# Performance work log

Hardware: AMD Instinct MI355X
Metric: run time of the kernel (lower is better)

## Reference

```python
import jax, jax.numpy as jnp
import numpy as np

B, S, D_MODEL, N_HEADS = 4, 2048, 512, 2
D4 = D_MODEL * 4            # output dim of quaternion projections (2048)
HD = D4 // N_HEADS          # per-head dim (1024)
EPS = 1e-6


def quat_linear(x, W, b):
    """Hamilton-product quaternion linear.
    x: [..., 4*in_q] (quaternions interleaved r,i,j,k)
    W: [4, out_q, in_q] components (r,i,j,k); b: [4*out_q]
    returns [..., 4*out_q]
    """
    xq = x.reshape(x.shape[:-1] + (-1, 4))
    xr, xi, xj, xk = xq[..., 0], xq[..., 1], xq[..., 2], xq[..., 3]
    Wr, Wi, Wj, Wk = W[0], W[1], W[2], W[3]
    m = lambda a, M: jnp.einsum('...i,oi->...o', a, M)
    o_r = m(xr, Wr) - m(xi, Wi) - m(xj, Wj) - m(xk, Wk)
    o_i = m(xr, Wi) + m(xi, Wr) + m(xj, Wk) - m(xk, Wj)
    o_j = m(xr, Wj) - m(xi, Wk) + m(xj, Wr) + m(xk, Wi)
    o_k = m(xr, Wk) + m(xi, Wj) - m(xj, Wi) + m(xk, Wr)
    out = jnp.stack([o_r, o_i, o_j, o_k], axis=-1)
    return out.reshape(out.shape[:-2] + (-1,)) + b


def setup_inputs() -> dict:
    rng = jax.random.key(0)
    ks = jax.random.split(rng, 12)
    def w(k, out_q, in_q):
        return jax.random.normal(k, (4, out_q, in_q), jnp.float32) * (1.0 / np.sqrt(4.0 * in_q))
    in_q_small = D_MODEL // 4   # q/k/v projections: d_model reals -> d_model quaternions
    in_q_big = D4 // 4          # later projections: 4*d_model reals -> d_model quaternions
    zb = jnp.zeros((D4,), jnp.float32)
    return {
        'query': jax.random.normal(ks[0], (B, S, D_MODEL), jnp.float32),
        'key':   jax.random.normal(ks[1], (B, S, D_MODEL), jnp.float32),
        'value': jax.random.normal(ks[2], (B, S, D_MODEL), jnp.float32),
        'Wq': w(ks[3], D_MODEL, in_q_small), 'bq': zb,
        'Wk': w(ks[4], D_MODEL, in_q_small), 'bk': zb,
        'Wv': w(ks[5], D_MODEL, in_q_small), 'bv': zb,
        'alpha': jax.random.normal(ks[6], (D4,), jnp.float32) * 0.1,
        'Wint': w(ks[7], D_MODEL, in_q_big), 'bint': zb,
        'Wfin': w(ks[8], D_MODEL, in_q_big), 'bfin': zb,
        'Wout': w(ks[9], D_MODEL, in_q_big), 'bout': zb,
    }


def reference(query, key, value, Wq, bq, Wk, bk, Wv, bv, alpha,
              Wint, bint, Wfin, bfin, Wout, bout):
    Q = quat_linear(query, Wq, bq).reshape(B, S, N_HEADS, HD)
    K = quat_linear(key, Wk, bk).reshape(B, S, N_HEADS, HD)
    V = quat_linear(value, Wv, bv).reshape(B, S, N_HEADS, HD)

    # spectral attention: FFT correlation + adaptive spectral filter
    Qf = jnp.fft.fft(Q, axis=1)
    Kf = jnp.fft.fft(K, axis=1)
    corr = Qf * jnp.conj(Kf)                        # [B,S,H,HD] complex64
    freqs = jnp.abs(jnp.fft.fftfreq(S))             # [S]
    phase = jnp.arctan(jnp.log(freqs + EPS))        # [S]
    a = alpha.reshape(N_HEADS, HD)
    filt = jnp.exp(1j * (phase[:, None, None] * a[None, :, :]))  # [S,H,HD]
    attn_w = jnp.fft.ifft(corr * filt[None], axis=1).real        # [B,S,H,HD]
    attn = (attn_w * V).reshape(B, S, -1)           # [B,S,4*d_model]

    attn = quat_linear(attn, Wint, bint)
    attn = quat_linear(attn, Wfin, bfin)
    return quat_linear(attn, Wout, bout)            # [B,S,4*d_model]
```

## Files before the change

kernel.cpp:

```cpp
#include <hip/hip_runtime.h>
#include <hip/hip_bf16.h>
#include <cstdint>

typedef unsigned short u16;
typedef u16  u16x8 __attribute__((ext_vector_type(8)));
typedef short s16x8 __attribute__((ext_vector_type(8)));
typedef float f32x4 __attribute__((ext_vector_type(4)));

#define PI_F 3.14159265358979323846f
#define PD(i) ((i) + 3 * ((i) >> 5))

static __device__ __forceinline__ u16 f2bf(float f) {
    union { float f; unsigned u; } v; v.f = f;
    unsigned r = v.u + 0x7fffu + ((v.u >> 16) & 1u);
    return (u16)(r >> 16);
}
static __device__ __forceinline__ float bf2f(u16 h) {
    union { unsigned u; float f; } v; v.u = ((unsigned)h) << 16;
    return v.f;
}

__device__ __forceinline__ void gl_lds16(const u16* g, u16* l) {
    __builtin_amdgcn_global_load_lds(
        (const __attribute__((address_space(1))) unsigned int*)g,
        (__attribute__((address_space(3))) unsigned int*)l, 16, 0, 0);
}

__device__ __forceinline__ void cvt_body(int blk, const float* __restrict__ in,
                                         u16* __restrict__ o) {
    int i = blk * 256 + threadIdx.x;
    float4 a = ((const float4*)in)[2 * i];
    float4 b = ((const float4*)in)[2 * i + 1];
    u16x8 vv;
    vv[0] = f2bf(a.x); vv[1] = f2bf(a.y); vv[2] = f2bf(a.z); vv[3] = f2bf(a.w);
    vv[4] = f2bf(b.x); vv[5] = f2bf(b.y); vv[6] = f2bf(b.z); vv[7] = f2bf(b.w);
    ((u16x8*)o)[i] = vv;
}

template<int LOGK>
__device__ __forceinline__ void e3_body(int blk, const float* __restrict__ W,
                                        u16* __restrict__ E) {
    const int K = 1 << LOGK;
    int idx = blk * 256 + threadIdx.x;
    int n = idx >> LOGK, k = idx & (K - 1);
    int o = n >> 2, c = n & 3, i = k >> 2, cp = k & 3;
    const int   qm[4][4] = {{0,1,2,3},{1,0,3,2},{2,3,0,1},{3,2,1,0}};
    const float qs[4][4] = {{1.f,-1.f,-1.f,-1.f},{1.f,1.f,1.f,-1.f},
                            {1.f,-1.f,1.f,1.f},{1.f,1.f,-1.f,1.f}};
    int in_q = K >> 2;
    float w = W[(size_t)qm[c][cp] * 512 * in_q + (size_t)o * in_q + i] * qs[c][cp];
    E[idx] = f2bf(w);
}

__device__ __forceinline__ void tabs_body(int blk, float2* __restrict__ gws,
                                          float* __restrict__ ph) {
    int i = blk * 256 + threadIdx.x;
    if (i < 292) {
        int off, denom;
        if (i < 4)       { off = 0;  denom = 16;   }
        else if (i < 36) { off = 4;  denom = 128;  }
        else             { off = 36; denom = 1024; }
        float a = (-PI_F) * (float)(i - off) / (float)denom;
        gws[i] = make_float2(cosf(a), sinf(a));
    }
    if (i <= 1024) {
        ph[i] = atanf(logf((float)i * (1.0f / 2048.0f) + 1e-6f));
    }
}

__global__ __launch_bounds__(256) void fat_prep(
        const float* __restrict__ query, const float* __restrict__ key,
        const float* __restrict__ value, u16* __restrict__ Acvt,
        const float* __restrict__ Wq, const float* __restrict__ Wk,
        const float* __restrict__ Wv, u16* __restrict__ Eq,
        u16* __restrict__ Ek, u16* __restrict__ Ev,
        const float* __restrict__ Wint, const float* __restrict__ Wfin,
        const float* __restrict__ Wout, u16* __restrict__ Eint,
        u16* __restrict__ Efin, u16* __restrict__ Eout,
        float2* __restrict__ gws, float* __restrict__ pht) {
    int b = blockIdx.x;
    if (b < 6144) {
        int ten = b >> 11, r = b & 2047;
        const float* in = (ten == 0) ? query : (ten == 1) ? key : value;
        cvt_body(r, in, Acvt + (size_t)ten * 8192 * 512);
    } else if (b < 18432) {
        int rb = b - 6144;
        int y = rb >> 12, r = rb & 4095;
        e3_body<9>(r, (y == 0) ? Wq : (y == 1) ? Wk : Wv,
                   (y == 0) ? Eq : (y == 1) ? Ek : Ev);
    } else if (b < 67584) {
        int rb = b - 18432;
        int y = rb >> 14, r = rb & 16383;
        e3_body<11>(r, (y == 0) ? Wint : (y == 1) ? Wfin : Wout,
                    (y == 0) ? Eint : (y == 1) ? Efin : Eout);
    } else {
        tabs_body(b - 67584, gws, pht);
    }
}

__global__ __launch_bounds__(256) void matvec_E(const float* __restrict__ v,
                                                const u16* __restrict__ E,
                                                const float* __restrict__ badd,
                                                float* __restrict__ out) {
    int n    = (blockIdx.x * 256 + threadIdx.x) >> 6;
    int lane = threadIdx.x & 63;
    if (n >= 2048) return;
    const u16* row = E + (size_t)n * 2048;
    float s = 0.f;
    for (int j = lane; j < 2048; j += 64) s += v[j] * bf2f(row[j]);
#pragma unroll
    for (int o = 32; o; o >>= 1) s += __shfl_down(s, o, 64);
    if (lane == 0) out[n] = s + badd[n];
}

template<int K, int OUTMODE, int NBY>
__device__ __forceinline__ void gemm_body(int bid, u16* As, u16* Bs,
                                          const u16* __restrict__ A,
                                          const u16* __restrict__ E,
                                          const float* __restrict__ bias,
                                          void* __restrict__ outp) {
    const int t    = threadIdx.x;
    const int lane = t & 63, wave = t >> 6;
    const int wr   = wave >> 1, wc = wave & 1;
    const int lr   = lane & 15, kg = lane >> 4;
    const int l7   = lr & 7;

    constexpr int SPX = (4 * (NBY / 4)) / 8;
    const int xcd = bid & 7, p = bid >> 3;
    const int st  = xcd * SPX + (p >> 4);
    const int w   = p & 15;
    const int bx  = (st & 3) * 4 + (w & 3);
    const int by  = (st >> 2) * 4 + (w >> 2);
    const int m0  = by * 128;
    const int n0  = bx * 128;

    f32x4 acc[4][4];
#pragma unroll
    for (int i = 0; i < 4; ++i)
#pragma unroll
        for (int j = 0; j < 4; ++j) acc[i][j] = (f32x4){0.f, 0.f, 0.f, 0.f};

    const int arow = wr * 64 + lr;
    const int brow = wc * 64 + lr;

    for (int k0 = 0; k0 < K; k0 += 64) {
#pragma unroll
        for (int c = 0; c < 4; ++c) {
            int idx = t + c * 256;
            int row = idx >> 3, sl = idx & 7;
            int gsl = sl ^ (row & 7);
            gl_lds16(A + (size_t)(m0 + row) * K + k0 + gsl * 8, &As[idx * 8]);
            gl_lds16(E + (size_t)(n0 + row) * K + k0 + gsl * 8, &Bs[idx * 8]);
        }
        __syncthreads();
#pragma unroll
        for (int ks = 0; ks < 2; ++ks) {
            const int slot = (ks * 4 + kg) ^ l7;
            s16x8 av[4], bv[4];
#pragma unroll
            for (int mi = 0; mi < 4; ++mi)
                av[mi] = *(const s16x8*)&As[(arow + mi * 16) * 64 + slot * 8];
#pragma unroll
            for (int ni = 0; ni < 4; ++ni)
                bv[ni] = *(const s16x8*)&Bs[(brow + ni * 16) * 64 + slot * 8];
#pragma unroll
            for (int mi = 0; mi < 4; ++mi)
#pragma unroll
                for (int ni = 0; ni < 4; ++ni)
                    acc[mi][ni] = __builtin_amdgcn_mfma_f32_16x16x32_bf16(
                        av[mi], bv[ni], acc[mi][ni], 0, 0, 0);
        }
        __syncthreads();
    }

#pragma unroll
    for (int ni = 0; ni < 4; ++ni) {
        int n = n0 + wc * 64 + ni * 16 + lr;
        float bvl = bias ? bias[n] : 0.0f;
#pragma unroll
        for (int mi = 0; mi < 4; ++mi) {
#pragma unroll
            for (int r = 0; r < 4; ++r) {
                int m = m0 + wr * 64 + mi * 16 + kg * 4 + r;
                float val = acc[mi][ni][r] + bvl;
                if constexpr (OUTMODE == 0) {
                    ((u16*)outp)[(size_t)m * 2048 + n] = f2bf(val);
                } else if constexpr (OUTMODE == 1) {
                    ((float*)outp)[(size_t)m * 2048 + n] = val;
                } else {
                    int b = m >> 11, s = m & 2047;
                    ((u16*)outp)[((size_t)b * 2048 + n) * 2048 + s] = f2bf(val);
                }
            }
        }
    }
}

template<int K, int OUTMODE, int NBY>
__global__ __launch_bounds__(256) void gemm2(const u16* __restrict__ A,
                                             const u16* __restrict__ E,
                                             const float* __restrict__ bias,
                                             void* __restrict__ outp) {
    __shared__ u16 As[128 * 64];
    __shared__ u16 Bs[128 * 64];
    gemm_body<K, OUTMODE, NBY>(blockIdx.x, As, Bs, A, E, bias, outp);
}

__global__ __launch_bounds__(256) void gemm_fatA(const u16* __restrict__ Aq,
                                                 const u16* __restrict__ Eq,
                                                 const float* __restrict__ bq,
                                                 void* __restrict__ Qt,
                                                 const u16* __restrict__ Ak,
                                                 const u16* __restrict__ Ek,
                                                 const float* __restrict__ bk,
                                                 void* __restrict__ Kt,
                                                 const u16* __restrict__ Efin,
                                                 const u16* __restrict__ EintT,
                                                 void* __restrict__ T1T) {
    __shared__ u16 As[128 * 64];
    __shared__ u16 Bs[128 * 64];
    int bid = blockIdx.x;
    if (bid < 256) {
        gemm_body<2048, 2, 16>(bid, As, Bs, Efin, EintT, nullptr, T1T);
    } else {
        int pid = bid - 256;
        if (pid < 1024)
            gemm_body<512, 2, 64>(pid, As, Bs, Aq, Eq, bq, Qt);
        else
            gemm_body<512, 2, 64>(pid - 1024, As, Bs, Ak, Ek, bk, Kt);
    }
}

template<int LH, int OFF>
__device__ __forceinline__ void r8pass(float* re, float* im,
                                       const float2* __restrict__ wt, int t) {
    constexpr int h = 1 << LH;
    __syncthreads();
    const int j  = t & (h - 1);
    const int i0 = ((t >> LH) << (LH + 3)) | j;
    const float2 w = wt[OFF + j];
    const float t2r = w.x * w.x - w.y * w.y;
    const float t2i = 2.f * w.x * w.y;
    const float t1r = t2r * t2r - t2i * t2i;
    const float t1i = 2.f * t2r * t2i;
    const float S = 0.70710678118654752f;
    const float Ac = S * (w.x + w.y);
    const float Bc = S * (w.y - w.x);

    float xr[8], xi[8];
    int p[8];
#pragma unroll
    for (int k = 0; k < 8; ++k) {
        p[k] = PD(i0 + k * h);
        xr[k] = re[p[k]]; xi[k] = im[p[k]];
    }
#pragma unroll
    for (int kp = 0; kp < 8; kp += 2) {
        float tr = t1r * xr[kp + 1] - t1i * xi[kp + 1];
        float ti = t1r * xi[kp + 1] + t1i * xr[kp + 1];
        float ar = xr[kp], ai = xi[kp];
        xr[kp] = ar + tr;     xi[kp] = ai + ti;
        xr[kp + 1] = ar - tr; xi[kp + 1] = ai - ti;
    }
#pragma unroll
    for (int q = 0; q < 2; ++q) {
        int b0 = q * 4;
        {
            float tr = t2r * xr[b0 + 2] - t2i * xi[b0 + 2];
            float ti = t2r * xi[b0 + 2] + t2i * xr[b0 + 2];
            float ar = xr[b0], ai = xi[b0];
            xr[b0] = ar + tr;     xi[b0] = ai + ti;
            xr[b0 + 2] = ar - tr; xi[b0 + 2] = ai - ti;
        }
        {
            float tr = t2i * xr[b0 + 3] + t2r * xi[b0 + 3];
            float ti = t2i * xi[b0 + 3] - t2r * xr[b0 + 3];
            float ar = xr[b0 + 1], ai = xi[b0 + 1];
            xr[b0 + 1] = ar + tr; xi[b0 + 1] = ai + ti;
            xr[b0 + 3] = ar - tr; xi[b0 + 3] = ai - ti;
        }
    }
    {
        float tr = w.x * xr[4] - w.y * xi[4];
        float ti = w.x * xi[4] + w.y * xr[4];
        float ar = xr[0], ai = xi[0];
        xr[0] = ar + tr; xi[0] = ai + ti;
        xr[4] = ar - tr; xi[4] = ai - ti;
    }
    {
        float tr = Ac * xr[5] - Bc * xi[5];
        float ti = Ac * xi[5] + Bc * xr[5];
        float ar = xr[1], ai = xi[1];
        xr[1] = ar + tr; xi[1] = ai + ti;
        xr[5] = ar - tr; xi[5] = ai - ti;
    }
    {
        float tr = w.y * xr[6] + w.x * xi[6];
        float ti = w.y * xi[6] - w.x * xr[6];
        float ar = xr[2], ai = xi[2];
        xr[2] = ar + tr; xi[2] = ai + ti;
        xr[6] = ar - tr; xi[6] = ai - ti;
    }
    {
        float tr = Bc * xr[7] + Ac * xi[7];
        float ti = Bc * xi[7] - Ac * xr[7];
        float ar = xr[3], ai = xi[3];
        xr[3] = ar + tr; xi[3] = ai + ti;
        xr[7] = ar - tr; xi[7] = ai - ti;
    }
#pragma unroll
    for (int k = 0; k < 8; ++k) { re[p[k]] = xr[k]; im[p[k]] = xi[k]; }
}

__device__ void fft2048(float* re, float* im, const float2* __restrict__ wt, int t) {
    __syncthreads();
#pragma unroll
    for (int u = 0; u < 2; ++u) {
        int i0 = (t + u * 256) << 2;
        int p0 = PD(i0);
        float x0r = re[p0],     x0i = im[p0];
        float x1r = re[p0 + 1], x1i = im[p0 + 1];
        float x2r = re[p0 + 2], x2i = im[p0 + 2];
        float x3r = re[p0 + 3], x3i = im[p0 + 3];
        float ar = x0r + x1r, ai = x0i + x1i;
        float br = x0r - x1r, bi = x0i - x1i;
        float cr = x2r + x3r, ci = x2i + x3i;
        float dr = x2r - x3r, di = x2i - x3i;
        re[p0]     = ar + cr; im[p0]     = ai + ci;
        re[p0 + 2] = ar - cr; im[p0 + 2] = ai - ci;
        re[p0 + 1] = br + di; im[p0 + 1] = bi - dr;
        re[p0 + 3] = br - di; im[p0 + 3] = bi + dr;
    }
    r8pass<2, 0>(re, im, wt, t);
    r8pass<5, 4>(re, im, wt, t);
    r8pass<8, 36>(re, im, wt, t);
    __syncthreads();
}

__device__ void spectral_body(int sbid, float* zre, float* zim, float2* wt,
                              const u16* __restrict__ Qt,
                              const u16* __restrict__ Kt,
                              u16* __restrict__ Wt,
                              const float* __restrict__ alpha,
                              const float2* __restrict__ gws,
                              const float* __restrict__ gph) {
    const int t  = threadIdx.x;
    const int b  = sbid >> 10;
    const int cp = sbid & 1023;
    const int c0 = cp * 2;
    const size_t base0 = ((size_t)b * 2048 + c0) * 2048;
    const size_t base1 = base0 + 2048;

    for (int i = t; i < 292; i += 256) wt[i] = gws[i];

    float ph[4];
    float PH1r[4], PH1i[4], PH2r[4], PH2i[4];
    float ph24 = 0.f, PH24_1 = 0.f, PH24_2 = 0.f;

#pragma unroll
    for (int ch = 0; ch < 2; ++ch) {
        const size_t base = ch ? base1 : base0;
        const u16* Qp = Qt + base;
        const u16* Kp = Kt + base;
        __syncthreads();
#pragma unroll
        for (int u = 0; u < 8; ++u) {
            int s = t + u * 256;
            int r = __brev((unsigned)s) >> 21;
            zre[PD(r)] = bf2f(Qp[s]);
            zim[PD(r)] = bf2f(Kp[s]);
        }
        fft2048(zre, zim, wt, t);
        const float ac = alpha[c0 + ch];
#pragma unroll
        for (int u = 0; u < 4; ++u) {
            int k = t + u * 256;
            int m = (2048 - k) & 2047;
            float ar = zre[PD(k)], ai = zim[PD(k)];
            float br = zre[PD(m)], bi = zim[PD(m)];
            float qr = 0.5f * (ar + br), qi = 0.5f * (ai - bi);
            float kr = 0.5f * (ai + bi), ki = 0.5f * (br - ar);
            float cr = qr * kr + qi * ki;
            float ci = qi * kr - qr * ki;
            if (ch == 0) ph[u] = gph[min(k, 2048 - k)];
            float fr, fi;
            __sincosf(ph[u] * ac, &fi, &fr);
            float Pkr = cr * fr - ci * fi, Pki = cr * fi + ci * fr;
            float qr2 = 0.5f * (br + ar), qi2 = 0.5f * (bi - ai);
            float kr2 = 0.5f * (bi + ai), ki2 = 0.5f * (ar - br);
            float cr2 = qr2 * kr2 + qi2 * ki2;
            float ci2 = qi2 * kr2 - qr2 * ki2;
            float Pmr = cr2 * fr - ci2 * fi, Pmi = cr2 * fi + ci2 * fr;
            float hr = 0.5f * (Pkr + Pmr), hi = 0.5f * (Pki - Pmi);
            if (ch == 0) { PH1r[u] = hr; PH1i[u] = hi; }
            else         { PH2r[u] = hr; PH2i[u] = hi; }
        }
        if (t == 0) {
            float ar = zre[PD(1024)], ai = zim[PD(1024)];
            float cr = ar * ai;
            if (ch == 0) ph24 = gph[1024];
            float fr, fi;
            __sincosf(ph24 * ac, &fi, &fr);
            if (ch == 0) PH24_1 = cr * fr; else PH24_2 = cr * fr;
        }
    }

    __syncthreads();
#pragma unroll
    for (int u = 0; u < 4; ++u) {
        int k = t + u * 256;
        int m = (2048 - k) & 2047;
        int rk = __brev((unsigned)k) >> 21;
        int rm = __brev((unsigned)m) >> 21;
        zre[PD(rk)] = PH1r[u] - PH2i[u];
        zim[PD(rk)] = PH1i[u] + PH2r[u];
        zre[PD(rm)] = PH1r[u] + PH2i[u];
        zim[PD(rm)] = PH2r[u] - PH1i[u];
    }
    if (t == 0) {
        zre[PD(1)] = PH24_1;
        zim[PD(1)] = PH24_2;
    }
    fft2048(zre, zim, wt, t);

#pragma unroll
    for (int u = 0; u < 8; ++u) {
        int s = t + u * 256;
        int j = (2048 - s) & 2047;
        Wt[base0 + s] = f2bf(zre[PD(j)] * (1.0f / 2048.0f));
        Wt[base1 + s] = f2bf(zim[PD(j)] * (1.0f / 2048.0f));
    }
}

__global__ __launch_bounds__(256) void fat_specv(const u16* __restrict__ Qt,
                                                 const u16* __restrict__ Kt,
                                                 u16* __restrict__ Wt,
                                                 const float* __restrict__ alpha,
                                                 const float2* __restrict__ gws,
                                                 const float* __restrict__ gph,
                                                 const u16* __restrict__ Av,
                                                 const u16* __restrict__ Ev,
                                                 const float* __restrict__ bvb,
                                                 void* __restrict__ Vt,
                                                 const u16* __restrict__ Eout,
                                                 const u16* __restrict__ T1T,
                                                 void* __restrict__ Ecomb) {
    __shared__ __align__(16) char smem[32768];
    int bid = blockIdx.x;
    if (bid < 256) {
        gemm_body<2048, 0, 16>(bid, (u16*)smem, (u16*)(smem + 16384),
                               Eout, T1T, nullptr, Ecomb);
        return;
    }
    bid -= 256;
    if (bid % 5 == 4) {
        gemm_body<512, 2, 64>(bid / 5, (u16*)smem, (u16*)(smem + 16384),
                              Av, Ev, bvb, Vt);
    } else {
        int sbid = (bid / 5) * 4 + (bid % 5);
        spectral_body(sbid, (float*)smem, (float*)(smem + 8960),
                      (float2*)(smem + 17920), Qt, Kt, Wt, alpha, gws, gph);
    }
}

__global__ __launch_bounds__(256) void transpose_k(const u16* __restrict__ in,
                                                   u16* __restrict__ out) {
    __shared__ u16 tile[32][33];
    int b = blockIdx.z;
    int c0 = blockIdx.x * 32, s0 = blockIdx.y * 32;
    int tx = threadIdx.x, ty = threadIdx.y;
#pragma unroll
    for (int dy = 0; dy < 32; dy += 8)
        tile[ty + dy][tx] = in[((size_t)b * 2048 + c0 + ty + dy) * 2048 + s0 + tx];
    __syncthreads();
#pragma unroll
    for (int dy = 0; dy < 32; dy += 8)
        out[((size_t)b * 2048 + s0 + ty + dy) * 2048 + c0 + tx] = tile[tx][ty + dy];
}

__global__ __launch_bounds__(256) void transpose_mul(const u16* __restrict__ W,
                                                     const u16* __restrict__ V,
                                                     u16* __restrict__ out) {
    __shared__ u16 tile[32][33];
    int b = blockIdx.z;
    int c0 = blockIdx.x * 32, s0 = blockIdx.y * 32;
    int tx = threadIdx.x, ty = threadIdx.y;
#pragma unroll
    for (int dy = 0; dy < 32; dy += 8) {
        size_t idx = ((size_t)b * 2048 + c0 + ty + dy) * 2048 + s0 + tx;
        tile[ty + dy][tx] = f2bf(bf2f(W[idx]) * bf2f(V[idx]));
    }
    __syncthreads();
#pragma unroll
    for (int dy = 0; dy < 32; dy += 8)
        out[((size_t)b * 2048 + s0 + ty + dy) * 2048 + c0 + tx] = tile[tx][ty + dy];
}

extern "C" void kernel_launch(void* const* d_in, const int* in_sizes, int n_in,
                              void* d_out, int out_size, void* d_ws, size_t ws_size,
                              hipStream_t stream) {
    const float* query = (const float*)d_in[0];
    const float* key   = (const float*)d_in[1];
    const float* value = (const float*)d_in[2];
    const float* Wq    = (const float*)d_in[3];
    const float* bq    = (const float*)d_in[4];
    const float* Wk    = (const float*)d_in[5];
    const float* bk    = (const float*)d_in[6];
    const float* Wv    = (const float*)d_in[7];
    const float* bv    = (const float*)d_in[8];
    const float* alpha = (const float*)d_in[9];
    const float* Wint  = (const float*)d_in[10];
    const float* bint  = (const float*)d_in[11];
    const float* Wfin  = (const float*)d_in[12];
    const float* bfin  = (const float*)d_in[13];
    const float* Wout  = (const float*)d_in[14];
    const float* bout  = (const float*)d_in[15];

    char* ws = (char*)d_ws;
    size_t off = 0;
    auto alloc = [&](size_t bytes) -> void* {
        void* p = ws + off;
        off += (bytes + 255) & ~(size_t)255;
        return p;
    };
    u16* Eq   = (u16*)alloc((size_t)2048 * 512 * 2);
    u16* Ek   = (u16*)alloc((size_t)2048 * 512 * 2);
    u16* Ev   = (u16*)alloc((size_t)2048 * 512 * 2);
    u16* Eint = (u16*)alloc((size_t)2048 * 2048 * 2);
    u16* Efin = (u16*)alloc((size_t)2048 * 2048 * 2);
    u16* Eout = (u16*)alloc((size_t)2048 * 2048 * 2);
    u16* EintT= (u16*)alloc((size_t)2048 * 2048 * 2);
    u16* T1T  = (u16*)alloc((size_t)2048 * 2048 * 2);
    u16* Qt   = (u16*)alloc((size_t)4 * 2048 * 2048 * 2);
    u16* Kt   = (u16*)alloc((size_t)4 * 2048 * 2048 * 2);
    u16* Vt   = (u16*)alloc((size_t)4 * 2048 * 2048 * 2);
    u16* attn = (u16*)alloc((size_t)8192 * 2048 * 2);
    float2* gws = (float2*)alloc(292 * 8);
    float*  pht = (float*)alloc(1025 * 4);
    float*  bv1 = (float*)alloc(2048 * 4);
    float*  bv2 = (float*)alloc(2048 * 4);
    u16* Ecomb = Eint;
    u16* Wt    = Qt;
    u16* Aq = attn;
    u16* Ak = attn + (size_t)8192 * 512;
    u16* Av = attn + (size_t)8192 * 1024;

    fat_prep<<<67589, 256, 0, stream>>>(query, key, value, Aq,
                                        Wq, Wk, Wv, Eq, Ek, Ev,
                                        Wint, Wfin, Wout, Eint, Efin, Eout,
                                        gws, pht);

    dim3 gt1(64, 64, 1);
    transpose_k<<<gt1, dim3(32, 8), 0, stream>>>(Eint, EintT);

    gemm_fatA<<<2304, 256, 0, stream>>>(Aq, Eq, bq, Qt, Ak, Ek, bk, Kt,
                                        Efin, EintT, T1T);

    matvec_E<<<512, 256, 0, stream>>>(bint, Efin, bfin, bv1);
    matvec_E<<<512, 256, 0, stream>>>(bv1,  Eout, bout, bv2);

    fat_specv<<<5376, 256, 0, stream>>>(Qt, Kt, Wt, alpha, gws, pht,
                                        Av, Ev, bv, Vt, Eout, T1T, Ecomb);

    dim3 gt(64, 64, 4);
    transpose_mul<<<gt, dim3(32, 8), 0, stream>>>(Wt, Vt, attn);

    gemm2<2048, 1, 64><<<1024, 256, 0, stream>>>(attn, Ecomb, bv2, (float*)d_out);
}
```

Baseline: 362.2 us.

## Fold bias matvecs into fat GEMM kernels and vectorize transpose_mul tiles

The two standalone matvec launches that fold biases through Efin and Eout now run as extra blocks appended to the gemm_fatA and fat_specv grids. Each matvec sits in the launch where its input is already available: bv1 needs only bint, and bv2 needs bv1 from the earlier kernel. This removes two kernel launches and lets the small matvecs overlap with the GEMM and spectral work. transpose_mul now uses 64x64 tiles with 4-wide u16 vector loads and stores, cutting memory transactions, though the LDS reads on the store side are strided.

```diff
diff --git a/kernel.cpp b/kernel.cpp
--- a/kernel.cpp
+++ b/kernel.cpp
@@ -3,6 +3,7 @@
 #include <cstdint>
 
 typedef unsigned short u16;
+typedef u16  u16x4 __attribute__((ext_vector_type(4)));
 typedef u16  u16x8 __attribute__((ext_vector_type(8)));
 typedef short s16x8 __attribute__((ext_vector_type(8)));
 typedef float f32x4 __attribute__((ext_vector_type(4)));
@@ -98,11 +99,11 @@
     }
 }
 
-__global__ __launch_bounds__(256) void matvec_E(const float* __restrict__ v,
-                                                const u16* __restrict__ E,
-                                                const float* __restrict__ badd,
-                                                float* __restrict__ out) {
-    int n    = (blockIdx.x * 256 + threadIdx.x) >> 6;
+__device__ __forceinline__ void mv_body(int blk, const float* __restrict__ v,
+                                        const u16* __restrict__ E,
+                                        const float* __restrict__ badd,
+                                        float* __restrict__ out) {
+    int n    = (blk * 256 + threadIdx.x) >> 6;
     int lane = threadIdx.x & 63;
     if (n >= 2048) return;
     const u16* row = E + (size_t)n * 2048;
@@ -216,18 +217,21 @@
                                                  void* __restrict__ Kt,
                                                  const u16* __restrict__ Efin,
                                                  const u16* __restrict__ EintT,
-                                                 void* __restrict__ T1T) {
+                                                 void* __restrict__ T1T,
+                                                 const float* __restrict__ bint,
+                                                 const float* __restrict__ bfin,
+                                                 float* __restrict__ bv1) {
     __shared__ u16 As[128 * 64];
     __shared__ u16 Bs[128 * 64];
     int bid = blockIdx.x;
     if (bid < 256) {
         gemm_body<2048, 2, 16>(bid, As, Bs, Efin, EintT, nullptr, T1T);
+    } else if (bid < 1280) {
+        gemm_body<512, 2, 64>(bid - 256, As, Bs, Aq, Eq, bq, Qt);
+    } else if (bid < 2304) {
+        gemm_body<512, 2, 64>(bid - 1280, As, Bs, Ak, Ek, bk, Kt);
     } else {
-        int pid = bid - 256;
-        if (pid < 1024)
-            gemm_body<512, 2, 64>(pid, As, Bs, Aq, Eq, bq, Qt);
-        else
-            gemm_body<512, 2, 64>(pid - 1024, As, Bs, Ak, Ek, bk, Kt);
+        mv_body(bid - 2304, bint, Efin, bfin, bv1);
     }
 }
 
@@ -444,12 +448,19 @@
                                                  void* __restrict__ Vt,
                                                  const u16* __restrict__ Eout,
                                                  const u16* __restrict__ T1T,
-                                                 void* __restrict__ Ecomb) {
+                                                 void* __restrict__ Ecomb,
+                                                 const float* __restrict__ bv1,
+                                                 const float* __restrict__ bout,
+                                                 float* __restrict__ bv2) {
     __shared__ __align__(16) char smem[32768];
     int bid = blockIdx.x;
     if (bid < 256) {
         gemm_body<2048, 0, 16>(bid, (u16*)smem, (u16*)(smem + 16384),
                                Eout, T1T, nullptr, Ecomb);
+        return;
+    }
+    if (bid >= 5376) {
+        mv_body(bid - 5376, bv1, Eout, bout, bv2);
         return;
     }
     bid -= 256;
@@ -481,19 +492,32 @@
 __global__ __launch_bounds__(256) void transpose_mul(const u16* __restrict__ W,
                                                      const u16* __restrict__ V,
                                                      u16* __restrict__ out) {
-    __shared__ u16 tile[32][33];
-    int b = blockIdx.z;
-    int c0 = blockIdx.x * 32, s0 = blockIdx.y * 32;
-    int tx = threadIdx.x, ty = threadIdx.y;
-#pragma unroll
-    for (int dy = 0; dy < 32; dy += 8) {
-        size_t idx = ((size_t)b * 2048 + c0 + ty + dy) * 2048 + s0 + tx;
-        tile[ty + dy][tx] = f2bf(bf2f(W[idx]) * bf2f(V[idx]));
+    __shared__ u16 tile[64][70];
+    const int b  = blockIdx.z;
+    const int c0 = blockIdx.x * 64, s0 = blockIdx.y * 64;
+    const int t  = threadIdx.x;
+    const int g  = (t & 15) * 4;
+    const int rb = t >> 4;
+
+#pragma unroll
+    for (int r = 0; r < 4; ++r) {
+        int c = rb + 16 * r;
+        size_t idx = ((size_t)b * 2048 + c0 + c) * 2048 + s0 + g;
+        u16x4 wv = *(const u16x4*)&W[idx];
+        u16x4 vv = *(const u16x4*)&V[idx];
+#pragma unroll
+        for (int j = 0; j < 4; ++j)
+            tile[c][g + j] = f2bf(bf2f(wv[j]) * bf2f(vv[j]));
     }
     __syncthreads();
 #pragma unroll
-    for (int dy = 0; dy < 32; dy += 8)
-        out[((size_t)b * 2048 + s0 + ty + dy) * 2048 + c0 + tx] = tile[tx][ty + dy];
+    for (int r = 0; r < 4; ++r) {
+        int s = rb + 16 * r;
+        u16x4 o;
+#pragma unroll
+        for (int j = 0; j < 4; ++j) o[j] = tile[g + j][s];
+        *(u16x4*)&out[((size_t)b * 2048 + s0 + s) * 2048 + c0 + g] = o;
+    }
 }
 
 extern "C" void kernel_launch(void* const* d_in, const int* in_sizes, int n_in,
@@ -553,17 +577,15 @@
     dim3 gt1(64, 64, 1);
     transpose_k<<<gt1, dim3(32, 8), 0, stream>>>(Eint, EintT);
 
-    gemm_fatA<<<2304, 256, 0, stream>>>(Aq, Eq, bq, Qt, Ak, Ek, bk, Kt,
-                                        Efin, EintT, T1T);
-
-    matvec_E<<<512, 256, 0, stream>>>(bint, Efin, bfin, bv1);
-    matvec_E<<<512, 256, 0, stream>>>(bv1,  Eout, bout, bv2);
-
-    fat_specv<<<5376, 256, 0, stream>>>(Qt, Kt, Wt, alpha, gws, pht,
-                                        Av, Ev, bv, Vt, Eout, T1T, Ecomb);
-
-    dim3 gt(64, 64, 4);
-    transpose_mul<<<gt, dim3(32, 8), 0, stream>>>(Wt, Vt, attn);
+    gemm_fatA<<<2816, 256, 0, stream>>>(Aq, Eq, bq, Qt, Ak, Ek, bk, Kt,
+                                        Efin, EintT, T1T, bint, bfin, bv1);
+
+    fat_specv<<<5888, 256, 0, stream>>>(Qt, Kt, Wt, alpha, gws, pht,
+                                        Av, Ev, bv, Vt, Eout, T1T, Ecomb,
+                                        bv1, bout, bv2);
+
+    dim3 gt(32, 32, 4);
+    transpose_mul<<<gt, 256, 0, stream>>>(Wt, Vt, attn);
 
     gemm2<2048, 1, 64><<<1024, 256, 0, stream>>>(attn, Ecomb, bv2, (float*)d_out);
 }
```

Result: faster. 354.2 us (-2.2%).
